# Optimization experiments

Measured on AMD Instinct MI355X. Metric: run time of the kernel, lower is better.

## Reference

```python
import jax, jax.numpy as jnp
import numpy as np

# ---- config constants (from init_kwargs) ----
NA = 2            # num anchors
NT = 5            # num consecutive frames
NDET = 2          # num_classes + 1
NREG = 6
X_MIN, X_MAX = 0.0, 64.0
Y_MIN, Y_MAX = -32.0, 32.0
CONF_THR = 0.7
ANCHORS = np.array([[3.9, 1.6], [1.0, 0.6]], dtype=np.float32)  # (a_l, a_w)


def setup_inputs() -> dict:
    key = jax.random.key(0)
    k1, k2 = jax.random.split(key)
    nB, nH, nW = 8, 320, 320
    out_detection = jax.random.normal(k1, (nB, NA * NDET * NT, nH, nW), dtype=jnp.float32)
    out_regression = jax.random.normal(k2, (nB, NA * NREG * NT, nH, nW), dtype=jnp.float32)
    return {"out_detection": out_detection, "out_regression": out_regression}


def reference(out_detection, out_regression):
    nB, _, nH, nW = out_detection.shape
    fov_h = X_MAX - X_MIN
    fov_w = Y_MAX - Y_MIN

    # (nB, nA, C, nT, nH, nW) -> (nB, nT, nA, nH, nW, C)
    det = out_detection.reshape(nB, NA, NDET, NT, nH, nW).transpose(0, 3, 1, 4, 5, 2)
    det = jax.nn.softmax(det, axis=-1)
    reg = out_regression.reshape(nB, NA, NREG, NT, nH, nW).transpose(0, 3, 1, 4, 5, 2)

    t_x = jax.nn.sigmoid(reg[..., 0]) * (fov_h / nH)
    t_y = jax.nn.sigmoid(reg[..., 1]) * (fov_w / nW)
    angle = jnp.arctan2(reg[..., 5], reg[..., 4])

    # grids replicate torch's repeat+view memory reinterpretation exactly
    grid_x = (jnp.tile(jnp.arange(nH, dtype=jnp.float32), nW)
              * (fov_h / nH)).reshape(1, 1, 1, nH, nW)
    grid_y = (jnp.tile(jnp.arange(-nW / 2, nW / 2, dtype=jnp.float32), nH)
              * (fov_w / nW)).reshape(1, 1, 1, nH, nW)

    anchors = jnp.asarray(ANCHORS)
    a_l = anchors[:, 0].reshape(1, 1, NA, 1, 1)
    a_w = anchors[:, 1].reshape(1, 1, NA, 1, 1)

    # torch fills reg_boxes from .data (detached); indices 2/3 swap t_l/t_w sources
    reg_boxes = jnp.stack([
        t_x + grid_x,                      # x
        t_y + grid_y,                      # y
        jnp.exp(reg[..., 3]) * a_l,        # l (from t_l = reg[...,3])
        jnp.exp(reg[..., 2]) * a_w,        # w (from t_w = reg[...,2])
        angle,                             # heading
    ], axis=-1)
    reg_boxes = jax.lax.stop_gradient(reg_boxes)

    object_prob = det[..., 1]  # (nB, nT, nA, nH, nW)
    best_anchor = jnp.argmax(object_prob, axis=2)  # max over anchor dim
    mask = (object_prob > CONF_THR) & (
        jnp.arange(NA).reshape(1, 1, NA, 1, 1) == best_anchor[:, :, None]
    )

    # Fixed-shape equivalent of the variable-length compaction: full (box, score)
    # tensor + boolean keep-mask; torch output == boxes_scores[mask] per (b, t).
    boxes_scores = jnp.concatenate([reg_boxes, object_prob[..., None]], axis=-1)
    return boxes_scores, mask
```

## Files before the change

kernel.cpp:

```cpp
#include <hip/hip_runtime.h>
#include <math.h>

constexpr int kNB   = 8;
constexpr int kNT   = 5;
constexpr int kNA   = 2;
constexpr int kNDET = 2;
constexpr int kNREG = 6;
constexpr int kNH   = 320;
constexpr int kNW   = 320;
constexpr int kHW   = kNH * kNW;
constexpr int kHW4  = kHW / 4;
constexpr int kDetCh = kNA * kNDET * kNT;
constexpr int kRegCh = kNA * kNREG * kNT;
constexpr int kBoxFloats = kNB * kNT * kNA * kHW * 6;
constexpr int kQuads = kNB * kNT * kHW4;
constexpr int kBlock = 256;
constexpr int kGrid  = kQuads / kBlock;

typedef float f32x4 __attribute__((ext_vector_type(4)));

__device__ __forceinline__ float sigmoidf_(float x) {
    return 1.0f / (1.0f + expf(-x));
}

__global__ __launch_bounds__(256) void fafe_predict(
    const float* __restrict__ det, const float* __restrict__ reg,
    float* __restrict__ out)
{
    __shared__ f32x4 lds4[6 * 256];
    float* ldsf = reinterpret_cast<float*>(lds4);

    const int tid = threadIdx.x;
    const int idx = blockIdx.x * kBlock + tid;
    const int q   = idx % kHW4;
    const int bt  = idx / kHW4;
    const int t   = bt % kNT;
    const int b   = bt / kNT;
    const int wb  = (q * 4) % kNW;
    const int qbase = q - tid;

    const float4* det4 = reinterpret_cast<const float4*>(det);
    const float4* reg4 = reinterpret_cast<const float4*>(reg);
    float4* out4 = reinterpret_cast<float4*>(out);

    constexpr int kPlane6o4  = kHW * 6 / 4;
    constexpr int kMaskBase4 = kBoxFloats / 4;

    const int dbase = (b * kDetCh + t) * kHW4 + q;
    const float4 d00 = det4[dbase + 0  * kHW4];
    const float4 d01 = det4[dbase + 5  * kHW4];
    const float4 d10 = det4[dbase + 10 * kHW4];
    const float4 d11 = det4[dbase + 15 * kHW4];

    float p0[4], p1[4];
    f32x4 m0v, m1v;
    {
        const float* x00 = reinterpret_cast<const float*>(&d00);
        const float* x01 = reinterpret_cast<const float*>(&d01);
        const float* x10 = reinterpret_cast<const float*>(&d10);
        const float* x11 = reinterpret_cast<const float*>(&d11);
#pragma unroll
        for (int j = 0; j < 4; ++j) {
            p0[j] = sigmoidf_(x01[j] - x00[j]);
            p1[j] = sigmoidf_(x11[j] - x10[j]);
            const bool best1 = p1[j] > p0[j];
            m0v[j] = (p0[j] > 0.7f && !best1) ? 1.0f : 0.0f;
            m1v[j] = (p1[j] > 0.7f && best1) ? 1.0f : 0.0f;
        }
    }
    __builtin_nontemporal_store(
        m0v, reinterpret_cast<f32x4*>(&out4[kMaskBase4 + (bt * 2 + 0) * kHW4 + q]));
    __builtin_nontemporal_store(
        m1v, reinterpret_cast<f32x4*>(&out4[kMaskBase4 + (bt * 2 + 1) * kHW4 + q]));

    const int rbase = (b * kRegCh + t) * kHW4 + q;
#pragma unroll
    for (int a = 0; a < kNA; ++a) {
        const int ab = rbase + a * 30 * kHW4;
        const float4 r0 = reg4[ab + 0  * kHW4];
        const float4 r1 = reg4[ab + 5  * kHW4];
        const float4 r2 = reg4[ab + 10 * kHW4];
        const float4 r3 = reg4[ab + 15 * kHW4];
        const float4 r4 = reg4[ab + 20 * kHW4];
        const float4 r5 = reg4[ab + 25 * kHW4];

        const float a_l = (a == 0) ? 3.9f : 1.0f;
        const float a_w = (a == 0) ? 1.6f : 0.6f;
        const float* pp = (a == 0) ? p0 : p1;

        const float* x0 = reinterpret_cast<const float*>(&r0);
        const float* x1 = reinterpret_cast<const float*>(&r1);
        const float* x2 = reinterpret_cast<const float*>(&r2);
        const float* x3 = reinterpret_cast<const float*>(&r3);
        const float* x4 = reinterpret_cast<const float*>(&r4);
        const float* x5 = reinterpret_cast<const float*>(&r5);

        f32x4 cx, cy, cl, cw, cg, cs;
#pragma unroll
        for (int j = 0; j < 4; ++j) {
            const float gw  = (float)(wb + j);
            const float gwm = gw - 160.0f;
            cx[j] = sigmoidf_(x0[j]) * 0.2f + gw  * 0.2f;
            cy[j] = sigmoidf_(x1[j]) * 0.2f + gwm * 0.2f;
            cl[j] = expf(x3[j]) * a_l;
            cw[j] = expf(x2[j]) * a_w;
            cg[j] = atan2f(x5[j], x4[j]);
            cs[j] = pp[j];
        }

        if (a == 1) __syncthreads();
        lds4[0 * 256 + tid] = cx;
        lds4[1 * 256 + tid] = cy;
        lds4[2 * 256 + tid] = cl;
        lds4[3 * 256 + tid] = cw;
        lds4[4 * 256 + tid] = cg;
        lds4[5 * 256 + tid] = cs;
        __syncthreads();

        const int obase = (bt * 2 + a) * kPlane6o4 + qbase * 6;
#pragma unroll
        for (int k = 0; k < 6; ++k) {
            const int o  = k * 256 + tid;
            const int f0 = 4 * o;
            f32x4 v;
#pragma unroll
            for (int e = 0; e < 4; ++e) {
                const int f = f0 + e;
                v[e] = ldsf[(f % 6) * 1024 + (f / 6)];
            }
            __builtin_nontemporal_store(
                v, reinterpret_cast<f32x4*>(&out4[obase + o]));
        }
    }
}

extern "C" void kernel_launch(void* const* d_in, const int* in_sizes, int n_in,
                              void* d_out, int out_size, void* d_ws, size_t ws_size,
                              hipStream_t stream) {
    const float* det = (const float*)d_in[0];
    const float* reg = (const float*)d_in[1];
    float* out = (float*)d_out;
    fafe_predict<<<kGrid, kBlock, 0, stream>>>(det, reg, out);
}
```

Before: 406.1 us.

## Hoist all regression loads and use per-wave LDS transpose without block barriers

```diff
diff --git a/kernel.cpp b/kernel.cpp
--- a/kernel.cpp
+++ b/kernel.cpp
@@ -27,17 +27,21 @@
     const float* __restrict__ det, const float* __restrict__ reg,
     float* __restrict__ out)
 {
-    __shared__ f32x4 lds4[6 * 256];
-    float* ldsf = reinterpret_cast<float*>(lds4);
+    __shared__ f32x4 lds4[4][6 * 64];
 
-    const int tid = threadIdx.x;
+    const int tid  = threadIdx.x;
+    const int wave = tid >> 6;
+    const int lane = tid & 63;
+    f32x4* wreg  = lds4[wave];
+    float* wregf = reinterpret_cast<float*>(wreg);
+
     const int idx = blockIdx.x * kBlock + tid;
     const int q   = idx % kHW4;
     const int bt  = idx / kHW4;
     const int t   = bt % kNT;
     const int b   = bt / kNT;
     const int wb  = (q * 4) % kNW;
-    const int qbase = q - tid;
+    const int wq  = q - lane;
 
     const float4* det4 = reinterpret_cast<const float4*>(det);
     const float4* reg4 = reinterpret_cast<const float4*>(reg);
@@ -51,6 +55,20 @@
     const float4 d01 = det4[dbase + 5  * kHW4];
     const float4 d10 = det4[dbase + 10 * kHW4];
     const float4 d11 = det4[dbase + 15 * kHW4];
+
+    const int rbase = (b * kRegCh + t) * kHW4 + q;
+    const float4 r00 = reg4[rbase + 0  * kHW4];
+    const float4 r01 = reg4[rbase + 5  * kHW4];
+    const float4 r02 = reg4[rbase + 10 * kHW4];
+    const float4 r03 = reg4[rbase + 15 * kHW4];
+    const float4 r04 = reg4[rbase + 20 * kHW4];
+    const float4 r05 = reg4[rbase + 25 * kHW4];
+    const float4 r10 = reg4[rbase + 30 * kHW4];
+    const float4 r11 = reg4[rbase + 35 * kHW4];
+    const float4 r12 = reg4[rbase + 40 * kHW4];
+    const float4 r13 = reg4[rbase + 45 * kHW4];
+    const float4 r14 = reg4[rbase + 50 * kHW4];
+    const float4 r15 = reg4[rbase + 55 * kHW4];
 
     float p0[4], p1[4];
     f32x4 m0v, m1v;
@@ -73,17 +91,14 @@
     __builtin_nontemporal_store(
         m1v, reinterpret_cast<f32x4*>(&out4[kMaskBase4 + (bt * 2 + 1) * kHW4 + q]));
 
-    const int rbase = (b * kRegCh + t) * kHW4 + q;
 #pragma unroll
     for (int a = 0; a < kNA; ++a) {
-        const int ab = rbase + a * 30 * kHW4;
-        const float4 r0 = reg4[ab + 0  * kHW4];
-        const float4 r1 = reg4[ab + 5  * kHW4];
-        const float4 r2 = reg4[ab + 10 * kHW4];
-        const float4 r3 = reg4[ab + 15 * kHW4];
-        const float4 r4 = reg4[ab + 20 * kHW4];
-        const float4 r5 = reg4[ab + 25 * kHW4];
-
+        const float4& r0 = (a == 0) ? r00 : r10;
+        const float4& r1 = (a == 0) ? r01 : r11;
+        const float4& r2 = (a == 0) ? r02 : r12;
+        const float4& r3 = (a == 0) ? r03 : r13;
+        const float4& r4 = (a == 0) ? r04 : r14;
+        const float4& r5 = (a == 0) ? r05 : r15;
         const float a_l = (a == 0) ? 3.9f : 1.0f;
         const float a_w = (a == 0) ? 1.6f : 0.6f;
         const float* pp = (a == 0) ? p0 : p1;
@@ -108,29 +123,29 @@
             cs[j] = pp[j];
         }
 
-        if (a == 1) __syncthreads();
-        lds4[0 * 256 + tid] = cx;
-        lds4[1 * 256 + tid] = cy;
-        lds4[2 * 256 + tid] = cl;
-        lds4[3 * 256 + tid] = cw;
-        lds4[4 * 256 + tid] = cg;
-        lds4[5 * 256 + tid] = cs;
-        __syncthreads();
+        wreg[0 * 64 + lane] = cx;
+        wreg[1 * 64 + lane] = cy;
+        wreg[2 * 64 + lane] = cl;
+        wreg[3 * 64 + lane] = cw;
+        wreg[4 * 64 + lane] = cg;
+        wreg[5 * 64 + lane] = cs;
+        __builtin_amdgcn_wave_barrier();
 
-        const int obase = (bt * 2 + a) * kPlane6o4 + qbase * 6;
+        const int obase = (bt * 2 + a) * kPlane6o4 + wq * 6;
 #pragma unroll
         for (int k = 0; k < 6; ++k) {
-            const int o  = k * 256 + tid;
+            const int o  = k * 64 + lane;
             const int f0 = 4 * o;
             f32x4 v;
 #pragma unroll
             for (int e = 0; e < 4; ++e) {
                 const int f = f0 + e;
-                v[e] = ldsf[(f % 6) * 1024 + (f / 6)];
+                v[e] = wregf[(f % 6) * 256 + (f / 6)];
             }
             __builtin_nontemporal_store(
                 v, reinterpret_cast<f32x4*>(&out4[obase + o]));
         }
+        __builtin_amdgcn_wave_barrier();
     }
 }
 
```

Result: no change. 410.7 us (+1.1%).
